# Optimization experiments

Hardware: AMD Instinct MI355X
Metric: run time of the kernel (lower is better)

The kernel has to match this reference:

```python
import jax, jax.numpy as jnp
import numpy as np

HEADS = 8
EPS = 1e-5


def _layernorm(x, g, b):
    mu = jnp.mean(x, axis=-1, keepdims=True)
    var = jnp.mean(jnp.square(x - mu), axis=-1, keepdims=True)
    return (x - mu) * jax.lax.rsqrt(var + EPS) * g + b


def setup_inputs() -> dict:
    key = jax.random.key(0)
    ks = jax.random.split(key, 10)
    B, S, D = 4, 2048, 256
    d_ff = 2 * D
    s = 0.02
    return {
        "x": jax.random.normal(ks[0], (B, S, D), dtype=jnp.float32),
        "ln1_g": jnp.ones((D,), jnp.float32),
        "ln1_b": jnp.zeros((D,), jnp.float32),
        "w_qkv": jax.random.normal(ks[1], (3 * D, D), jnp.float32) * s,
        "b_qkv": jnp.zeros((3 * D,), jnp.float32),
        "w_proj": jax.random.normal(ks[2], (D, D), jnp.float32) * s,
        "b_proj": jnp.zeros((D,), jnp.float32),
        "ln2_g": jnp.ones((D,), jnp.float32),
        "ln2_b": jnp.zeros((D,), jnp.float32),
        "w1": jax.random.normal(ks[3], (d_ff, D), jnp.float32) * s,
        "b1": jnp.zeros((d_ff,), jnp.float32),
        "w2": jax.random.normal(ks[4], (D, d_ff), jnp.float32) * s,
        "b2": jnp.zeros((D,), jnp.float32),
    }


def reference(x, ln1_g, ln1_b, w_qkv, b_qkv, w_proj, b_proj,
              ln2_g, ln2_b, w1, b1, w2, b2):
    B, S, D = x.shape
    H = HEADS
    dh = D // H
    scale = dh ** -0.5

    # --- attention sublayer (pre-LN) ---
    y = _layernorm(x, ln1_g, ln1_b)
    qkv = y @ w_qkv.T + b_qkv                       # [B,S,3D]
    qkv = qkv.reshape(B, S, 3, H, dh)
    q = jnp.transpose(qkv[:, :, 0], (0, 2, 1, 3))   # [B,H,S,dh]
    k = jnp.transpose(qkv[:, :, 1], (0, 2, 1, 3))
    v = jnp.transpose(qkv[:, :, 2], (0, 2, 1, 3))
    attn = jax.nn.softmax(jnp.einsum('bhsd,bhtd->bhst', q, k) * scale, axis=-1)
    ctx = jnp.einsum('bhst,bhtd->bhsd', attn, v)    # [B,H,S,dh]
    ctx = jnp.transpose(ctx, (0, 2, 1, 3)).reshape(B, S, D)
    x = x + ctx @ w_proj.T + b_proj

    # --- FFN sublayer (pre-LN) ---
    y = _layernorm(x, ln2_g, ln2_b)
    h = jax.nn.silu(y @ w1.T + b1)                  # [B,S,2D]
    x = x + h @ w2.T + b2
    return x
```

## Files before the change

kernel.cpp:

```cpp
#include <hip/hip_runtime.h>
#include <cstddef>

constexpr int kB   = 4;
constexpr int kS   = 2048;
constexpr int kD   = 256;
constexpr int kH   = 8;
constexpr int kDH  = 32;
constexpr int kDFF = 512;
constexpr int kM   = kB * kS;
constexpr float kEps = 1e-5f;
constexpr float kScaleL2E = 0.17677669529663687f * 1.4426950408889634f;

typedef float f32x4  __attribute__((ext_vector_type(4)));
typedef short bf16x8 __attribute__((ext_vector_type(8)));
typedef unsigned short u16;
typedef unsigned int   u32;

__device__ inline u16 f2bf(float x) {
    union { float f; unsigned u; } c; c.f = x;
    const unsigned r = c.u + 0x7fffu + ((c.u >> 16) & 1u);
    return (u16)(r >> 16);
}

__device__ inline u32 pk_trunc(float lo, float hi) {
    union { float f; u32 u; } a, b; a.f = lo; b.f = hi;
    return __builtin_amdgcn_perm(b.u, a.u, 0x07060302u);
}

__device__ inline size_t pkoff(int row, int col, int nkb) {
    return ((size_t)(row >> 4) * nkb + (col >> 5)) * 512
         + (row & 15) * 32 + (col & 31);
}

__global__ __launch_bounds__(256)
void prep_kernel(const float* __restrict__ x, const float* __restrict__ g,
                 const float* __restrict__ b, u16* __restrict__ y,
                 const float* __restrict__ wq, const float* __restrict__ wp,
                 const float* __restrict__ w1, const float* __restrict__ w2,
                 u16* __restrict__ wdst)
{
    if (blockIdx.x >= kM / 4) {
        const int e0 = ((blockIdx.x - kM / 4) * 256 + threadIdx.x) * 4;
        const float* src; int off, K, base;
        if (e0 < 196608)      { src = wq; off = e0;          K = 256; base = 0; }
        else if (e0 < 262144) { src = wp; off = e0 - 196608; K = 256; base = 196608; }
        else if (e0 < 393216) { src = w1; off = e0 - 262144; K = 256; base = 262144; }
        else                  { src = w2; off = e0 - 393216; K = 512; base = 393216; }
        const float4 v = *(const float4*)&src[off];
        const int n = off / K, k = off - n * K;
        const size_t po = pkoff(n, k, K >> 5);
        *(ushort4*)&wdst[base + po] =
            make_ushort4(f2bf(v.x), f2bf(v.y), f2bf(v.z), f2bf(v.w));
        return;
    }
    const int wave = threadIdx.x >> 6;
    const int lane = threadIdx.x & 63;
    const int row  = blockIdx.x * 4 + wave;
    const float4 v = *(const float4*)&x[(size_t)row * kD + lane * 4];
    float s1 = (v.x + v.y) + (v.z + v.w);
    float s2 = (v.x * v.x + v.y * v.y) + (v.z * v.z + v.w * v.w);
    #pragma unroll
    for (int off = 1; off < 64; off <<= 1) {
        s1 += __shfl_xor(s1, off);
        s2 += __shfl_xor(s2, off);
    }
    const float mu  = s1 * (1.0f / kD);
    const float var = s2 * (1.0f / kD) - mu * mu;
    const float inv = rsqrtf(var + kEps);
    const float4 g4 = *(const float4*)&g[lane * 4];
    const float4 b4 = *(const float4*)&b[lane * 4];
    *(ushort4*)&y[pkoff(row, lane * 4, kD >> 5)] = make_ushort4(
        f2bf((v.x - mu) * inv * g4.x + b4.x),
        f2bf((v.y - mu) * inv * g4.y + b4.y),
        f2bf((v.z - mu) * inv * g4.z + b4.z),
        f2bf((v.w - mu) * inv * g4.w + b4.w));
}

template<int NI, int OUTMODE, bool RES, int KTOT>
__global__ __launch_bounds__(256)
void gemm_pk(const u16* __restrict__ Ap, const u16* __restrict__ Wp,
             const float* __restrict__ bias, const float* __restrict__ res,
             float* __restrict__ Cf, u16* __restrict__ Cb,
             u16* __restrict__ KbP, u16* __restrict__ VtP, int N)
{
    constexpr int NK = KTOT / 32;
    const int tid  = threadIdx.x;
    const int wave = tid >> 6;
    const int lane = tid & 63;
    const int quad = lane >> 4;
    const int l16  = lane & 15;
    const int m0 = blockIdx.x * 128;
    const int n0 = blockIdx.y * (NI * 16);
    const int fo = l16 * 32 + quad * 8;

    f32x4 acc[2][NI];
    #pragma unroll
    for (int mt = 0; mt < 2; ++mt)
        #pragma unroll
        for (int ni = 0; ni < NI; ++ni) acc[mt][ni] = {0.f, 0.f, 0.f, 0.f};

    const u16* a0p = Ap + (size_t)((m0 >> 4) + wave)     * NK * 512 + fo;
    const u16* a1p = Ap + (size_t)((m0 >> 4) + 4 + wave) * NK * 512 + fo;
    const u16* wp  = Wp + (size_t)(n0 >> 4)              * NK * 512 + fo;

    #pragma unroll 2
    for (int k = 0; k < NK; ++k) {
        const bf16x8 a0 = *(const bf16x8*)&a0p[k * 512];
        const bf16x8 a1 = *(const bf16x8*)&a1p[k * 512];
        #pragma unroll
        for (int ni = 0; ni < NI; ++ni) {
            const bf16x8 wf = *(const bf16x8*)&wp[((size_t)ni * NK + k) * 512];
            acc[0][ni] = __builtin_amdgcn_mfma_f32_16x16x32_bf16(a0, wf, acc[0][ni], 0, 0, 0);
            acc[1][ni] = __builtin_amdgcn_mfma_f32_16x16x32_bf16(a1, wf, acc[1][ni], 0, 0, 0);
        }
    }

    #pragma unroll
    for (int mt = 0; mt < 2; ++mt) {
        #pragma unroll
        for (int ni = 0; ni < NI; ++ni) {
            const float bias_v = bias[n0 + ni * 16 + l16];
            #pragma unroll
            for (int r = 0; r < 4; ++r) {
                const int m = m0 + mt * 64 + wave * 16 + quad * 4 + r;
                const int n = n0 + ni * 16 + l16;
                float v = acc[mt][ni][r] + bias_v;
                if (OUTMODE == 0) {
                    if (RES) v += res[(size_t)m * N + n];
                    Cf[(size_t)m * N + n] = v;
                } else if (OUTMODE == 1) {
                    v = v / (1.0f + __expf(-v));
                    Cb[pkoff(m, n, kDFF >> 5)] = f2bf(v);
                } else {
                    const int rgn = n0 >> 8;
                    const int nl  = n & 255;
                    const int hh  = nl >> 5, dh = nl & 31;
                    const int bb  = m >> 11, s = m & (kS - 1);
                    const int bh  = bb * kH + hh;
                    if (rgn == 0)
                        Cb[((size_t)bh * kS + s) * kDH + dh] = f2bf(v * kScaleL2E);
                    else if (rgn == 1)
                        KbP[((size_t)bh * kS + s) * kDH + dh] = f2bf(v);
                    else {
                        const int so = s & 31;
                        const int vq = (so >> 2) & 3;
                        const int vj = (so & 3) | (((so >> 4) & 1) << 2);
                        VtP[(((size_t)bh * (kS / 32) + (s >> 5)) * 4 + vq) * 256
                            + dh * 8 + vj] = f2bf(v);
                    }
                }
            }
        }
    }
}

__global__ __launch_bounds__(256)
void proj_ln2_kernel(const u16* __restrict__ ctx, const u16* __restrict__ Wp,
                     const float* __restrict__ bias, const float* __restrict__ x,
                     const float* __restrict__ g, const float* __restrict__ bb,
                     float* __restrict__ out, u16* __restrict__ y)
{
    const int tid  = threadIdx.x;
    const int wave = tid >> 6;
    const int lane = tid & 63;
    const int quad = lane >> 4;
    const int l16  = lane & 15;
    const int tr   = blockIdx.x * 4 + wave;
    const int fo   = l16 * 32 + quad * 8;

    f32x4 acc[16];
    #pragma unroll
    for (int ni = 0; ni < 16; ++ni) acc[ni] = {0.f, 0.f, 0.f, 0.f};

    const u16* ap = ctx + (size_t)tr * 8 * 512 + fo;
    #pragma unroll 2
    for (int k = 0; k < 8; ++k) {
        const bf16x8 a = *(const bf16x8*)&ap[k * 512];
        #pragma unroll
        for (int ni = 0; ni < 16; ++ni) {
            const bf16x8 wf = *(const bf16x8*)&Wp[((size_t)ni * 8 + k) * 512 + fo];
            acc[ni] = __builtin_amdgcn_mfma_f32_16x16x32_bf16(a, wf, acc[ni], 0, 0, 0);
        }
    }

    float bv[16], gv[16], bbv[16];
    #pragma unroll
    for (int ni = 0; ni < 16; ++ni) {
        bv[ni]  = bias[ni * 16 + l16];
        gv[ni]  = g[ni * 16 + l16];
        bbv[ni] = bb[ni * 16 + l16];
    }

    const int m0 = tr * 16;
    #pragma unroll
    for (int r = 0; r < 4; ++r) {
        const int m = m0 + quad * 4 + r;
        float v[16], s1 = 0.f, s2 = 0.f;
        #pragma unroll
        for (int ni = 0; ni < 16; ++ni) {
            v[ni] = acc[ni][r] + bv[ni] + x[(size_t)m * kD + ni * 16 + l16];
            out[(size_t)m * kD + ni * 16 + l16] = v[ni];
            s1 += v[ni];
            s2 += v[ni] * v[ni];
        }
        s1 += __shfl_xor(s1, 1); s2 += __shfl_xor(s2, 1);
        s1 += __shfl_xor(s1, 2); s2 += __shfl_xor(s2, 2);
        s1 += __shfl_xor(s1, 4); s2 += __shfl_xor(s2, 4);
        s1 += __shfl_xor(s1, 8); s2 += __shfl_xor(s2, 8);
        const float mu  = s1 * (1.0f / kD);
        const float var = s2 * (1.0f / kD) - mu * mu;
        const float inv = rsqrtf(var + kEps);
        u16* yb = y + (size_t)tr * 8 * 512 + (quad * 4 + r) * 32 + l16;
        #pragma unroll
        for (int ni = 0; ni < 16; ++ni)
            yb[(ni >> 1) * 512 + (ni & 1) * 16] =
                f2bf((v[ni] - mu) * inv * gv[ni] + bbv[ni]);
    }
}

__global__ __launch_bounds__(256)
void attn_kernel(const u16* __restrict__ Qb, const u16* __restrict__ Kb,
                 const u16* __restrict__ Vp, u16* __restrict__ ctx)
{
    __shared__ float cbuf[2][64 * 33];
    const int tid  = threadIdx.x;
    const int wave = tid >> 6;
    const int lane = tid & 63;
    const int quad = lane >> 4;
    const int l16  = lane & 15;
    const int h = blockIdx.y;
    const int b = blockIdx.z;
    const int bh = b * kH + h;
    const int qsub = wave >> 1;
    const int half = wave & 1;
    const int q0 = blockIdx.x * 128 + qsub * 64;

    bf16x8 aq[4];
    #pragma unroll
    for (int qb = 0; qb < 4; ++qb)
        aq[qb] = *(const bf16x8*)
            &Qb[((size_t)bh * kS + q0 + qb * 16 + l16) * kDH + quad * 8];

    const u16* Kbase = Kb + (size_t)bh * kS * kDH;
    const u16* Vbase = Vp + (size_t)bh * (kS * 32);

    f32x4 O[4][2] = {};
    f32x4 lsum[4] = {};
    const f32x4 zz = {0.f, 0.f, 0.f, 0.f};
    union { u32 u[4]; bf16x8 v; } ones;
    ones.u[0] = ones.u[1] = ones.u[2] = ones.u[3] = 0x3F803F80u;

    auto load_tile = [&](int kt, bf16x8 (&kf)[4], bf16x8 (&vf)[2][2]) {
        #pragma unroll
        for (int kg = 0; kg < 4; ++kg)
            kf[kg] = *(const bf16x8*)
                &Kbase[(size_t)(kt + kg * 16 + l16) * kDH + quad * 8];
        #pragma unroll
        for (int ks = 0; ks < 2; ++ks)
            #pragma unroll
            for (int nf = 0; nf < 2; ++nf)
                vf[ks][nf] = *(const bf16x8*)
                    &Vbase[(size_t)(((kt >> 5) + ks) * 4 + quad) * 1024
                           + (nf * 16 + l16) * 8];
    };

    auto comp_tile = [&](bf16x8 (&kf)[4], bf16x8 (&vf)[2][2]) {
        #pragma unroll
        for (int qb = 0; qb < 4; ++qb) {
            f32x4 S0 = __builtin_amdgcn_mfma_f32_16x16x32_bf16(kf[0], aq[qb], zz, 0, 0, 0);
            f32x4 S1 = __builtin_amdgcn_mfma_f32_16x16x32_bf16(kf[1], aq[qb], zz, 0, 0, 0);
            f32x4 S2 = __builtin_amdgcn_mfma_f32_16x16x32_bf16(kf[2], aq[qb], zz, 0, 0, 0);
            f32x4 S3 = __builtin_amdgcn_mfma_f32_16x16x32_bf16(kf[3], aq[qb], zz, 0, 0, 0);

            union { u32 u[4]; bf16x8 v; } pA0, pA1;
            pA0.u[0] = pk_trunc(__builtin_amdgcn_exp2f(S0[0]), __builtin_amdgcn_exp2f(S0[1]));
            pA0.u[1] = pk_trunc(__builtin_amdgcn_exp2f(S0[2]), __builtin_amdgcn_exp2f(S0[3]));
            pA0.u[2] = pk_trunc(__builtin_amdgcn_exp2f(S1[0]), __builtin_amdgcn_exp2f(S1[1]));
            pA0.u[3] = pk_trunc(__builtin_amdgcn_exp2f(S1[2]), __builtin_amdgcn_exp2f(S1[3]));
            pA1.u[0] = pk_trunc(__builtin_amdgcn_exp2f(S2[0]), __builtin_amdgcn_exp2f(S2[1]));
            pA1.u[1] = pk_trunc(__builtin_amdgcn_exp2f(S2[2]), __builtin_amdgcn_exp2f(S2[3]));
            pA1.u[2] = pk_trunc(__builtin_amdgcn_exp2f(S3[0]), __builtin_amdgcn_exp2f(S3[1]));
            pA1.u[3] = pk_trunc(__builtin_amdgcn_exp2f(S3[2]), __builtin_amdgcn_exp2f(S3[3]));

            lsum[qb] = __builtin_amdgcn_mfma_f32_16x16x32_bf16(pA0.v, ones.v, lsum[qb], 0, 0, 0);
            lsum[qb] = __builtin_amdgcn_mfma_f32_16x16x32_bf16(pA1.v, ones.v, lsum[qb], 0, 0, 0);

            O[qb][0] = __builtin_amdgcn_mfma_f32_16x16x32_bf16(pA0.v, vf[0][0], O[qb][0], 0, 0, 0);
            O[qb][1] = __builtin_amdgcn_mfma_f32_16x16x32_bf16(pA0.v, vf[0][1], O[qb][1], 0, 0, 0);
            O[qb][0] = __builtin_amdgcn_mfma_f32_16x16x32_bf16(pA1.v, vf[1][0], O[qb][0], 0, 0, 0);
            O[qb][1] = __builtin_amdgcn_mfma_f32_16x16x32_bf16(pA1.v, vf[1][1], O[qb][1], 0, 0, 0);
        }
    };

    const int kbeg = half * (kS / 2);
    #pragma unroll 1
    for (int t2 = 0; t2 < 8; ++t2) {
        const int ktA = kbeg + t2 * 128;
        bf16x8 kfA[4], vfA[2][2], kfB[4], vfB[2][2];
        load_tile(ktA,      kfA, vfA);
        load_tile(ktA + 64, kfB, vfB);
        comp_tile(kfA, vfA);
        comp_tile(kfB, vfB);
    }

    float* cb = cbuf[qsub];
    if (half == 1) {
        #pragma unroll
        for (int qb = 0; qb < 4; ++qb)
            #pragma unroll
            for (int r = 0; r < 4; ++r) {
                const int row = qb * 16 + quad * 4 + r;
                cb[row * 33 + l16]      = O[qb][0][r];
                cb[row * 33 + 16 + l16] = O[qb][1][r];
                if (l16 == 0)
                    cb[row * 33 + 32] = lsum[qb][r];
            }
    }
    __syncthreads();
    if (half == 0) {
        #pragma unroll
        for (int qb = 0; qb < 4; ++qb)
            #pragma unroll
            for (int r = 0; r < 4; ++r) {
                const int row = qb * 16 + quad * 4 + r;
                const float lq  = lsum[qb][r] + cb[row * 33 + 32];
                const float inv = 1.0f / lq;
                const float o0 = O[qb][0][r] + cb[row * 33 + l16];
                const float o1 = O[qb][1][r] + cb[row * 33 + 16 + l16];
                const int q = q0 + row;
                const int mrow = b * kS + q;
                u16* crow = ctx + ((size_t)(mrow >> 4) * (kD >> 5) + h) * 512
                          + (mrow & 15) * 32;
                crow[l16]      = f2bf(o0 * inv);
                crow[16 + l16] = f2bf(o1 * inv);
            }
    }
}

extern "C" void kernel_launch(void* const* d_in, const int* in_sizes, int n_in,
                              void* d_out, int out_size, void* d_ws, size_t ws_size,
                              hipStream_t stream)
{
    const float* x      = (const float*)d_in[0];
    const float* ln1_g  = (const float*)d_in[1];
    const float* ln1_b  = (const float*)d_in[2];
    const float* w_qkv  = (const float*)d_in[3];
    const float* b_qkv  = (const float*)d_in[4];
    const float* w_proj = (const float*)d_in[5];
    const float* b_proj = (const float*)d_in[6];
    const float* ln2_g  = (const float*)d_in[7];
    const float* ln2_b  = (const float*)d_in[8];
    const float* w1     = (const float*)d_in[9];
    const float* b1     = (const float*)d_in[10];
    const float* w2     = (const float*)d_in[11];
    const float* b2     = (const float*)d_in[12];
    float* out = (float*)d_out;

    char* ws = (char*)d_ws;
    u16* Qb  = (u16*)ws;
    u16* Kb  = (u16*)(ws + ((size_t)4  << 20));
    u16* Vp  = (u16*)(ws + ((size_t)8  << 20));
    u16* ctx = (u16*)(ws + ((size_t)12 << 20));
    u16* y   = (u16*)(ws + ((size_t)16 << 20));
    u16* h   = (u16*)ws;
    u16* Wb  = (u16*)(ws + ((size_t)20 << 20));
    u16* wqb = Wb;
    u16* wpb = Wb + 196608;
    u16* w1b = Wb + 262144;
    u16* w2b = Wb + 393216;

    const dim3 blk(256);

    prep_kernel<<<dim3(kM / 4 + 512), blk, 0, stream>>>(
        x, ln1_g, ln1_b, y, w_qkv, w_proj, w1, w2, Wb);
    gemm_pk<4, 2, false, 256><<<dim3(kM / 128, 12), blk, 0, stream>>>(
        y, wqb, b_qkv, nullptr, nullptr, Qb, Kb, Vp, 0);
    attn_kernel<<<dim3(kS / 128, kH, kB), blk, 0, stream>>>(Qb, Kb, Vp, ctx);
    proj_ln2_kernel<<<dim3(kM / 64), blk, 0, stream>>>(
        ctx, wpb, b_proj, x, ln2_g, ln2_b, out, y);
    gemm_pk<4, 1, false, 256><<<dim3(kM / 128, kDFF / 64), blk, 0, stream>>>(
        y, w1b, b1, nullptr, nullptr, h, nullptr, nullptr, kDFF);
    gemm_pk<2, 0, true, 512><<<dim3(kM / 128, kD / 32), blk, 0, stream>>>(
        h, w2b, b2, out, out, nullptr, nullptr, nullptr, kD);
}
```

Baseline: 162.4 us.

## Switch GEMM and proj kernels to single-wave blocks with one 16-row tile each

The GEMM and proj+LN2 kernels now run as one 64-thread wave per block. Each wave computes a single 16-row M tile, where before a 256-thread block had each wave compute two 16-row tiles. The grid grows to many more small blocks, which should improve scheduling granularity and occupancy across CUs. The FFN2 GEMM also changes from NI=2 to NI=4. The cost is less reuse of the weight fragments loaded per wave, since each W fragment now feeds one MFMA instead of two, so weight load traffic roughly doubles.

```diff
diff --git a/kernel.cpp b/kernel.cpp
--- a/kernel.cpp
+++ b/kernel.cpp
@@ -77,95 +77,83 @@
 }
 
 template<int NI, int OUTMODE, bool RES, int KTOT>
-__global__ __launch_bounds__(256)
-void gemm_pk(const u16* __restrict__ Ap, const u16* __restrict__ Wp,
+__global__ __launch_bounds__(64)
+void gemm_1w(const u16* __restrict__ Ap, const u16* __restrict__ Wp,
              const float* __restrict__ bias, const float* __restrict__ res,
              float* __restrict__ Cf, u16* __restrict__ Cb,
              u16* __restrict__ KbP, u16* __restrict__ VtP, int N)
 {
     constexpr int NK = KTOT / 32;
-    const int tid  = threadIdx.x;
-    const int wave = tid >> 6;
-    const int lane = tid & 63;
+    const int lane = threadIdx.x & 63;
     const int quad = lane >> 4;
     const int l16  = lane & 15;
-    const int m0 = blockIdx.x * 128;
-    const int n0 = blockIdx.y * (NI * 16);
-    const int fo = l16 * 32 + quad * 8;
-
-    f32x4 acc[2][NI];
-    #pragma unroll
-    for (int mt = 0; mt < 2; ++mt)
-        #pragma unroll
-        for (int ni = 0; ni < NI; ++ni) acc[mt][ni] = {0.f, 0.f, 0.f, 0.f};
-
-    const u16* a0p = Ap + (size_t)((m0 >> 4) + wave)     * NK * 512 + fo;
-    const u16* a1p = Ap + (size_t)((m0 >> 4) + 4 + wave) * NK * 512 + fo;
-    const u16* wp  = Wp + (size_t)(n0 >> 4)              * NK * 512 + fo;
+    const int mt0  = blockIdx.x;
+    const int n0   = blockIdx.y * (NI * 16);
+    const int fo   = l16 * 32 + quad * 8;
+
+    f32x4 acc[NI];
+    #pragma unroll
+    for (int ni = 0; ni < NI; ++ni) acc[ni] = {0.f, 0.f, 0.f, 0.f};
+
+    const u16* ap = Ap + (size_t)mt0 * NK * 512 + fo;
+    const u16* wp = Wp + (size_t)(n0 >> 4) * NK * 512 + fo;
 
     #pragma unroll 2
     for (int k = 0; k < NK; ++k) {
-        const bf16x8 a0 = *(const bf16x8*)&a0p[k * 512];
-        const bf16x8 a1 = *(const bf16x8*)&a1p[k * 512];
+        const bf16x8 a = *(const bf16x8*)&ap[(size_t)k * 512];
         #pragma unroll
         for (int ni = 0; ni < NI; ++ni) {
             const bf16x8 wf = *(const bf16x8*)&wp[((size_t)ni * NK + k) * 512];
-            acc[0][ni] = __builtin_amdgcn_mfma_f32_16x16x32_bf16(a0, wf, acc[0][ni], 0, 0, 0);
-            acc[1][ni] = __builtin_amdgcn_mfma_f32_16x16x32_bf16(a1, wf, acc[1][ni], 0, 0, 0);
-        }
-    }
-
-    #pragma unroll
-    for (int mt = 0; mt < 2; ++mt) {
-        #pragma unroll
-        for (int ni = 0; ni < NI; ++ni) {
-            const float bias_v = bias[n0 + ni * 16 + l16];
-            #pragma unroll
-            for (int r = 0; r < 4; ++r) {
-                const int m = m0 + mt * 64 + wave * 16 + quad * 4 + r;
-                const int n = n0 + ni * 16 + l16;
-                float v = acc[mt][ni][r] + bias_v;
-                if (OUTMODE == 0) {
-                    if (RES) v += res[(size_t)m * N + n];
-                    Cf[(size_t)m * N + n] = v;
-                } else if (OUTMODE == 1) {
-                    v = v / (1.0f + __expf(-v));
-                    Cb[pkoff(m, n, kDFF >> 5)] = f2bf(v);
-                } else {
-                    const int rgn = n0 >> 8;
-                    const int nl  = n & 255;
-                    const int hh  = nl >> 5, dh = nl & 31;
-                    const int bb  = m >> 11, s = m & (kS - 1);
-                    const int bh  = bb * kH + hh;
-                    if (rgn == 0)
-                        Cb[((size_t)bh * kS + s) * kDH + dh] = f2bf(v * kScaleL2E);
-                    else if (rgn == 1)
-                        KbP[((size_t)bh * kS + s) * kDH + dh] = f2bf(v);
-                    else {
-                        const int so = s & 31;
-                        const int vq = (so >> 2) & 3;
-                        const int vj = (so & 3) | (((so >> 4) & 1) << 2);
-                        VtP[(((size_t)bh * (kS / 32) + (s >> 5)) * 4 + vq) * 256
-                            + dh * 8 + vj] = f2bf(v);
-                    }
+            acc[ni] = __builtin_amdgcn_mfma_f32_16x16x32_bf16(a, wf, acc[ni], 0, 0, 0);
+        }
+    }
+
+    #pragma unroll
+    for (int ni = 0; ni < NI; ++ni) {
+        const float bias_v = bias[n0 + ni * 16 + l16];
+        #pragma unroll
+        for (int r = 0; r < 4; ++r) {
+            const int m = mt0 * 16 + quad * 4 + r;
+            const int n = n0 + ni * 16 + l16;
+            float v = acc[ni][r] + bias_v;
+            if (OUTMODE == 0) {
+                if (RES) v += res[(size_t)m * N + n];
+                Cf[(size_t)m * N + n] = v;
+            } else if (OUTMODE == 1) {
+                v = v / (1.0f + __expf(-v));
+                Cb[pkoff(m, n, kDFF >> 5)] = f2bf(v);
+            } else {
+                const int rgn = n0 >> 8;
+                const int nl  = n & 255;
+                const int hh  = nl >> 5, dh = nl & 31;
+                const int bb  = m >> 11, s = m & (kS - 1);
+                const int bh  = bb * kH + hh;
+                if (rgn == 0)
+                    Cb[((size_t)bh * kS + s) * kDH + dh] = f2bf(v * kScaleL2E);
+                else if (rgn == 1)
+                    KbP[((size_t)bh * kS + s) * kDH + dh] = f2bf(v);
+                else {
+                    const int so = s & 31;
+                    const int vq = (so >> 2) & 3;
+                    const int vj = (so & 3) | (((so >> 4) & 1) << 2);
+                    VtP[(((size_t)bh * (kS / 32) + (s >> 5)) * 4 + vq) * 256
+                        + dh * 8 + vj] = f2bf(v);
                 }
             }
         }
     }
 }
 
-__global__ __launch_bounds__(256)
+__global__ __launch_bounds__(64)
 void proj_ln2_kernel(const u16* __restrict__ ctx, const u16* __restrict__ Wp,
                      const float* __restrict__ bias, const float* __restrict__ x,
                      const float* __restrict__ g, const float* __restrict__ bb,
                      float* __restrict__ out, u16* __restrict__ y)
 {
-    const int tid  = threadIdx.x;
-    const int wave = tid >> 6;
-    const int lane = tid & 63;
+    const int lane = threadIdx.x & 63;
     const int quad = lane >> 4;
     const int l16  = lane & 15;
-    const int tr   = blockIdx.x * 4 + wave;
+    const int tr   = blockIdx.x;
     const int fo   = l16 * 32 + quad * 8;
 
     f32x4 acc[16];
@@ -369,17 +357,15 @@
     u16* w1b = Wb + 262144;
     u16* w2b = Wb + 393216;
 
-    const dim3 blk(256);
-
-    prep_kernel<<<dim3(kM / 4 + 512), blk, 0, stream>>>(
+    prep_kernel<<<dim3(kM / 4 + 512), dim3(256), 0, stream>>>(
         x, ln1_g, ln1_b, y, w_qkv, w_proj, w1, w2, Wb);
-    gemm_pk<4, 2, false, 256><<<dim3(kM / 128, 12), blk, 0, stream>>>(
+    gemm_1w<4, 2, false, 256><<<dim3(kM / 16, 12), dim3(64), 0, stream>>>(
         y, wqb, b_qkv, nullptr, nullptr, Qb, Kb, Vp, 0);
-    attn_kernel<<<dim3(kS / 128, kH, kB), blk, 0, stream>>>(Qb, Kb, Vp, ctx);
-    proj_ln2_kernel<<<dim3(kM / 64), blk, 0, stream>>>(
+    attn_kernel<<<dim3(kS / 128, kH, kB), dim3(256), 0, stream>>>(Qb, Kb, Vp, ctx);
+    proj_ln2_kernel<<<dim3(kM / 16), dim3(64), 0, stream>>>(
         ctx, wpb, b_proj, x, ln2_g, ln2_b, out, y);
-    gemm_pk<4, 1, false, 256><<<dim3(kM / 128, kDFF / 64), blk, 0, stream>>>(
+    gemm_1w<4, 1, false, 256><<<dim3(kM / 16, kDFF / 64), dim3(64), 0, stream>>>(
         y, w1b, b1, nullptr, nullptr, h, nullptr, nullptr, kDFF);
-    gemm_pk<2, 0, true, 512><<<dim3(kM / 128, kD / 32), blk, 0, stream>>>(
+    gemm_1w<4, 0, true, 512><<<dim3(kM / 16, kD / 64), dim3(64), 0, stream>>>(
         h, w2b, b2, out, out, nullptr, nullptr, nullptr, kD);
 }
```

Measured after the change: 168.9 us. 4.0% more time.
